# Performance work log

Hardware: AMD Instinct MI355X
Metric: run time of the kernel (lower is better)

## Reference

```python
import jax, jax.numpy as jnp
import numpy as np

# ---- static config (matches init_kwargs) ----
NLAT, NLON = 181, 360
LMAX = NLAT                 # hard_thresholding_fraction = 1.0
MMAX = NLON // 2 + 1        # 181, real FFT in longitude
INC = 26
OUTC = 26
EMBED = 256
NLAYERS = 4
MLP_HID = int(EMBED * 2.0)
EPS = 1e-6


def _legendre(lmax, mmax, theta):
    """Orthonormal associated Legendre functions Pbar[l, m, k] at colatitudes theta."""
    ct, st = np.cos(theta), np.sin(theta)
    K = theta.size
    P = np.zeros((lmax, mmax, K), dtype=np.float64)
    P[0, 0] = np.sqrt(1.0 / (4.0 * np.pi))
    for m in range(1, mmax):
        P[m, m] = -np.sqrt((2.0 * m + 1.0) / (2.0 * m)) * st * P[m - 1, m - 1]
    for m in range(mmax):
        if m + 1 < lmax:
            P[m + 1, m] = np.sqrt(2.0 * m + 3.0) * ct * P[m, m]
        for l in range(m + 2, lmax):
            a = np.sqrt((4.0 * l * l - 1.0) / (l * l - m * m))
            b = np.sqrt(((2.0 * l + 1.0) * (l - 1.0 + m) * (l - 1.0 - m)) / ((2.0 * l - 3.0) * (l * l - m * m)))
            P[l, m] = a * ct * P[l - 1, m] - b * P[l - 2, m]
    return P

# equiangular grid + quadrature weights; precompute analysis/synthesis matrices
_theta = np.linspace(0.0, np.pi, NLAT)
_wq = (np.pi / (NLAT - 1)) * np.sin(_theta)
_P = _legendre(LMAX, MMAX, _theta)
PW = jnp.asarray((_P * (2.0 * np.pi * _wq)[None, None, :]).astype(np.float32))  # analysis
PS = jnp.asarray(_P.astype(np.float32))                                         # synthesis


def _ln(x):
    # per-pixel layer norm over channel dim, no affine (affine_norms=False)
    mu = jnp.mean(x, axis=1, keepdims=True)
    var = jnp.mean((x - mu) ** 2, axis=1, keepdims=True)
    return (x - mu) * jax.lax.rsqrt(var + EPS)


def _conv1x1(x, w, b=None):
    y = jnp.einsum('oi,bihw->bohw', w, x)
    return y if b is None else y + b[None, :, None, None]


def _sht(x):
    # x: (b,c,nlat,nlon) -> coeff (b,c,l,m) complex64
    F = jnp.fft.rfft(x, axis=-1) / NLON          # (b,c,k,m)
    return jnp.einsum('lmk,bckm->bclm', PW, F)


def _isht(c):
    F = jnp.einsum('lmk,bclm->bckm', PS, c)      # (b,c,k,m)
    return jnp.fft.irfft(F * NLON, n=NLON, axis=-1)


def _block(x, wsp, bsp, wis, bis, wf1, bf1, wf2, bf2):
    xn = _ln(x)                                  # norm0
    c = _sht(xn)
    co = jnp.einsum('oil,bilm->bolm', wsp, c)    # dhconv: diagonal in m, dense per l
    y = _isht(co) + bsp[None, :, None, None]
    x1 = y + _conv1x1(xn, wis, bis)              # inner linear skip (residual = filter input)
    x1 = jax.nn.gelu(x1, approximate=False)
    x2 = _ln(x1)                                 # norm1
    h = jax.nn.gelu(_conv1x1(x2, wf1, bf1), approximate=False)
    x2 = _conv1x1(h, wf2, bf2)                   # MLP
    return x2 + xn                               # outer identity skip


def setup_inputs() -> dict:
    key = jax.random.key(0)
    ks = jax.random.split(key, 10)
    n = jax.random.normal
    x = n(ks[0], (1, INC, NLAT, NLON), jnp.float32)
    w_enc = n(ks[1], (EMBED, INC), jnp.float32) * float(1.0 / np.sqrt(INC))
    b_enc = jnp.zeros((EMBED,), jnp.float32)
    pos_emb = n(ks[2], (1, EMBED, NLAT, NLON), jnp.float32) * 0.02
    w_spec = n(ks[3], (NLAYERS, EMBED, EMBED, LMAX), jnp.float32) * float(1.0 / np.sqrt(EMBED))
    b_spec = jnp.zeros((NLAYERS, EMBED), jnp.float32)
    w_iskip = n(ks[4], (NLAYERS, EMBED, EMBED), jnp.float32) * float(1.0 / np.sqrt(EMBED))
    b_iskip = jnp.zeros((NLAYERS, EMBED), jnp.float32)
    w_fc1 = n(ks[5], (NLAYERS, MLP_HID, EMBED), jnp.float32) * float(1.0 / np.sqrt(EMBED))
    b_fc1 = jnp.zeros((NLAYERS, MLP_HID), jnp.float32)
    w_fc2 = n(ks[6], (NLAYERS, EMBED, MLP_HID), jnp.float32) * float(1.0 / np.sqrt(MLP_HID))
    b_fc2 = jnp.zeros((NLAYERS, EMBED), jnp.float32)
    w_dec = n(ks[7], (OUTC, EMBED + INC), jnp.float32) * float(1.0 / np.sqrt(EMBED + INC))
    b_dec = jnp.zeros((OUTC,), jnp.float32)
    return {'x': x, 'w_enc': w_enc, 'b_enc': b_enc, 'pos_emb': pos_emb,
            'w_spec': w_spec, 'b_spec': b_spec, 'w_iskip': w_iskip, 'b_iskip': b_iskip,
            'w_fc1': w_fc1, 'b_fc1': b_fc1, 'w_fc2': w_fc2, 'b_fc2': b_fc2,
            'w_dec': w_dec, 'b_dec': b_dec}


def reference(x, w_enc, b_enc, pos_emb, w_spec, b_spec, w_iskip, b_iskip,
              w_fc1, b_fc1, w_fc2, b_fc2, w_dec, b_dec):
    res = x                                       # big_skip residual (raw input)
    h = _conv1x1(x, w_enc, b_enc) + pos_emb       # encoder + pos embed
    for i in range(NLAYERS):
        h = _block(h, w_spec[i], b_spec[i], w_iskip[i], b_iskip[i],
                   w_fc1[i], b_fc1[i], w_fc2[i], b_fc2[i])
    h = jnp.concatenate([h, res], axis=1)         # big skip concat
    return _conv1x1(h, w_dec, b_dec)
```

## Files before the change

kernel.cpp:

```cpp
#include <hip/hip_runtime.h>
#include <math.h>

#define NLATg 181
#define NLONg 360
#define PIXg  65160
#define EMBg  256
#define MHIDg 512
#define PLANEg 8386816
#define LDIMg 32761

#define FLAG_GELU 1
#define FLAG_ACC  2

__device__ __forceinline__ float gelu_f(float x) {
    return 0.5f * x * (1.0f + erff(x * 0.70710678118654752440f));
}


__global__ __launch_bounds__(256) void init_legendre(float* __restrict__ P) {
    int idx = blockIdx.x * 256 + threadIdx.x;
    if (idx >= 181 * 181) return;
    int m = idx / 181, k = idx % 181;
    double theta = M_PI * (double)k / 180.0;
    double ct = cos(theta), st = sin(theta);
    double pmm = sqrt(1.0 / (4.0 * M_PI));
    for (int j = 1; j <= m; ++j) pmm *= -sqrt((2.0 * j + 1.0) / (2.0 * j)) * st;
    for (int l = 0; l < m; ++l) P[(size_t)l * LDIMg + m * 181 + k] = 0.0f;
    P[(size_t)m * LDIMg + m * 181 + k] = (float)pmm;
    if (m + 1 < 181) {
        double pl1 = sqrt(2.0 * m + 3.0) * ct * pmm;
        P[(size_t)(m + 1) * LDIMg + m * 181 + k] = (float)pl1;
        double pl2 = pmm;
        for (int l = m + 2; l < 181; ++l) {
            double ll = l, mm = m;
            double a = sqrt((4.0 * ll * ll - 1.0) / (ll * ll - mm * mm));
            double b = sqrt(((2.0 * ll + 1.0) * (ll - 1.0 + mm) * (ll - 1.0 - mm)) /
                            ((2.0 * ll - 3.0) * (ll * ll - mm * mm)));
            double p = a * ct * pl1 - b * pl2;
            P[(size_t)l * LDIMg + m * 181 + k] = (float)p;
            pl2 = pl1; pl1 = p;
        }
    }
}

__global__ __launch_bounds__(256) void init_trig(float* __restrict__ Etrig,
                                                 float* __restrict__ Dt, float* __restrict__ wqs) {
    int idx = blockIdx.x * 256 + threadIdx.x;
    if (idx < 181) {
        double theta = M_PI * (double)idx / 180.0;
        wqs[idx] = (float)(2.0 * M_PI * (M_PI / 180.0) * sin(theta) / 360.0);
    }
    if (idx >= 181 * 360) return;
    int m = idx / 360, n = idx % 360;
    int a = (m * n) % 360;
    double ang = M_PI * (double)a / 180.0;
    double c = cos(ang), s = sin(ang);
    Etrig[idx]         = (float)c;
    Etrig[PIXg + idx]  = (float)(-s);
    double cm = (m == 0 || m == 180) ? 1.0 : 2.0;
    Dt[(size_t)m * 360 + n]         = (float)(cm * c);
    Dt[(size_t)(181 + m) * 360 + n] = (float)(-cm * s);
}

__global__ __launch_bounds__(256) void transpose_wspec(const float* __restrict__ W, float* __restrict__ WT) {
    __shared__ float tile[32][33];
    int l0 = blockIdx.x * 32, o0 = blockIdx.y * 32, i = blockIdx.z;
    int c = threadIdx.x & 31, r = threadIdx.x >> 5;
#pragma unroll
    for (int j = 0; j < 4; j++) {
        int row = r + j * 8;
        float v = 0.f;
        if (l0 + c < 181) v = W[(size_t)(o0 + row) * 46336 + i * 181 + (l0 + c)];
        tile[row][c] = v;
    }
    __syncthreads();
#pragma unroll
    for (int j = 0; j < 4; j++) {
        int row = r + j * 8;
        if (l0 + row < 181) WT[(size_t)(l0 + row) * 65536 + i * 256 + (o0 + c)] = tile[c][row];
    }
}

__global__ __launch_bounds__(256) void ln_kernel(const float* __restrict__ X, float* __restrict__ Y) {
    int p0 = blockIdx.x * 64;
    int t = threadIdx.x;
    int ps = t & 63, cg = t >> 6;
    int p = p0 + ps;
    bool ok = p < PIXg;
    float sum = 0.f, sumsq = 0.f;
    if (ok) {
        for (int c = cg; c < EMBg; c += 4) {
            float v = X[(size_t)c * PIXg + p];
            sum += v; sumsq += v * v;
        }
    }
    __shared__ float s1[4][64];
    __shared__ float s2[4][64];
    s1[cg][ps] = sum; s2[cg][ps] = sumsq;
    __syncthreads();
    float tot  = s1[0][ps] + s1[1][ps] + s1[2][ps] + s1[3][ps];
    float tot2 = s2[0][ps] + s2[1][ps] + s2[2][ps] + s2[3][ps];
    float mu = tot * (1.0f / 256.0f);
    float var = tot2 * (1.0f / 256.0f) - mu * mu;
    float inv = rsqrtf(var + 1e-6f);
    if (ok) {
        for (int c = cg; c < EMBg; c += 4) {
            size_t offp = (size_t)c * PIXg + p;
            Y[offp] = (X[offp] - mu) * inv;
        }
    }
}

__global__ __launch_bounds__(256) void add_bias_gelu(const float* __restrict__ Y, const float* __restrict__ S,
                                                     const float* __restrict__ bsp, float* __restrict__ O) {
    int idx = blockIdx.x * 256 + threadIdx.x;
    int c = idx / 16290;
    float b = bsp[c];
    float4 y = reinterpret_cast<const float4*>(Y)[idx];
    float4 s = reinterpret_cast<const float4*>(S)[idx];
    float4 o;
    o.x = gelu_f(y.x + s.x + b);
    o.y = gelu_f(y.y + s.y + b);
    o.z = gelu_f(y.z + s.z + b);
    o.w = gelu_f(y.w + s.w + b);
    reinterpret_cast<float4*>(O)[idx] = o;
}

__global__ __launch_bounds__(256, 2) void gemm_f32(
    const float* __restrict__ A, int Ars, int Acs, int Azs, int Aps,
    const float* __restrict__ B, int Brs, int Bcs, int Bzs, int Bps,
    float* __restrict__ C, int Crs, int Ccs, int Czs, int Cps,
    const float* __restrict__ bias, const float* __restrict__ zscale,
    const float* __restrict__ resid,
    int M, int N, int K, int Zin, int flags)
{
    int z = blockIdx.z;
    if (z >= Zin) { z -= Zin; A += Aps; B += Bps; C += Cps; if (resid) resid += Cps; }
    A += (size_t)z * Azs; B += (size_t)z * Bzs; C += (size_t)z * Czs;
    if (resid) resid += (size_t)z * Czs;

    const int bm = blockIdx.y * 128, bn = blockIdx.x * 128;
    const int t = threadIdx.x;
    const int tx = t & 15, ty = t >> 4;

    __shared__ float As[16][132];
    __shared__ float Bs[16][132];

    float acc[8][8];
#pragma unroll
    for (int i = 0; i < 8; i++)
#pragma unroll
        for (int j = 0; j < 8; j++) acc[i][j] = 0.0f;

    for (int k0 = 0; k0 < K; k0 += 16) {
        if (Acs == 1) {
            int kk = t & 15, r = t >> 4;
            int gk = k0 + kk; bool kv = gk < K;
#pragma unroll
            for (int i = 0; i < 8; i++) {
                int gr = bm + r + i * 16; if (gr > M - 1) gr = M - 1;
                As[kk][r + i * 16] = kv ? A[(size_t)gr * Ars + gk] : 0.f;
            }
        } else {
            int row = t & 127, kb = t >> 7;
            int gr = bm + row; if (gr > M - 1) gr = M - 1;
            size_t base = (size_t)gr * Ars;
#pragma unroll
            for (int i = 0; i < 8; i++) {
                int gk = k0 + kb + i * 2;
                As[kb + i * 2][row] = (gk < K) ? A[base + (size_t)gk * Acs] : 0.f;
            }
        }
        if (Bcs == 1) {
            int col = t & 127, kb = t >> 7;
            int gc = bn + col; if (gc > N - 1) gc = N - 1;
#pragma unroll
            for (int i = 0; i < 8; i++) {
                int gk = k0 + kb + i * 2;
                Bs[kb + i * 2][col] = (gk < K) ? B[(size_t)gk * Brs + gc] : 0.f;
            }
        } else {
            int kk = t & 15, cb = t >> 4;
            int gk = k0 + kk; bool kv = gk < K;
#pragma unroll
            for (int i = 0; i < 8; i++) {
                int gc = bn + cb + i * 16; if (gc > N - 1) gc = N - 1;
                Bs[kk][cb + i * 16] = kv ? B[(size_t)gk * Brs + (size_t)gc * Bcs] : 0.f;
            }
        }
        __syncthreads();
#pragma unroll
        for (int kk = 0; kk < 16; kk++) {
            float4 a0 = *(const float4*)&As[kk][ty * 4];
            float4 a1 = *(const float4*)&As[kk][ty * 4 + 64];
            float4 b0 = *(const float4*)&Bs[kk][tx * 4];
            float4 b1 = *(const float4*)&Bs[kk][tx * 4 + 64];
            float av[8] = {a0.x, a0.y, a0.z, a0.w, a1.x, a1.y, a1.z, a1.w};
            float bv[8] = {b0.x, b0.y, b0.z, b0.w, b1.x, b1.y, b1.z, b1.w};
#pragma unroll
            for (int i = 0; i < 8; i++)
#pragma unroll
                for (int j = 0; j < 8; j++)
                    acc[i][j] = fmaf(av[i], bv[j], acc[i][j]);
        }
        __syncthreads();
    }

    const float zs = zscale ? zscale[z] : 1.0f;
    const bool fastN = (Ccs == 1) && (bn + 128 <= N);
#pragma unroll
    for (int i = 0; i < 8; i++) {
        int gi = bm + ty * 4 + (i & 3) + ((i >> 2) << 6);
        if (gi >= M) continue;
        float bval = bias ? bias[gi] : 0.0f;
        size_t crow = (size_t)gi * (size_t)Crs;
        if (fastN) {
#pragma unroll
            for (int h = 0; h < 2; h++) {
                int gj = bn + tx * 4 + h * 64;
                size_t off = crow + (size_t)gj;
                float4 v;
                v.x = acc[i][h * 4 + 0] * zs + bval;
                v.y = acc[i][h * 4 + 1] * zs + bval;
                v.z = acc[i][h * 4 + 2] * zs + bval;
                v.w = acc[i][h * 4 + 3] * zs + bval;
                if (resid) { float4 r = *(const float4*)&resid[off];
                             v.x += r.x; v.y += r.y; v.z += r.z; v.w += r.w; }
                if (flags & FLAG_GELU) { v.x = gelu_f(v.x); v.y = gelu_f(v.y);
                                         v.z = gelu_f(v.z); v.w = gelu_f(v.w); }
                if (flags & FLAG_ACC)  { float4 c0 = *(const float4*)&C[off];
                                         v.x += c0.x; v.y += c0.y; v.z += c0.z; v.w += c0.w; }
                *(float4*)&C[off] = v;
            }
        } else {
#pragma unroll
            for (int j = 0; j < 8; j++) {
                int gj = bn + tx * 4 + (j & 3) + ((j >> 2) << 6);
                if (gj >= N) continue;
                size_t off = crow + (size_t)gj * (size_t)Ccs;
                float v = acc[i][j] * zs + bval;
                if (resid) v += resid[off];
                if (flags & FLAG_GELU) v = gelu_f(v);
                if (flags & FLAG_ACC) v += C[off];
                C[off] = v;
            }
        }
    }
}

static inline void launch_gemm(hipStream_t s,
    const float* A, int Ars, int Acs, int Azs, int Aps,
    const float* B, int Brs, int Bcs, int Bzs, int Bps,
    float* C, int Crs, int Ccs, int Czs, int Cps,
    const float* bias, const float* zscale, const float* resid,
    int M, int N, int K, int Zin, int nplanes, int flags)
{
    dim3 grid((N + 127) / 128, (M + 127) / 128, Zin * nplanes);
    hipLaunchKernelGGL(gemm_f32, grid, dim3(256), 0, s,
                       A, Ars, Acs, Azs, Aps, B, Brs, Bcs, Bzs, Bps,
                       C, Crs, Ccs, Czs, Cps, bias, zscale, resid,
                       M, N, K, Zin, flags);
}

extern "C" void kernel_launch(void* const* d_in, const int* in_sizes, int n_in,
                              void* d_out, int out_size, void* d_ws, size_t ws_size,
                              hipStream_t stream)
{
    const float* x      = (const float*)d_in[0];
    const float* w_enc  = (const float*)d_in[1];
    const float* b_enc  = (const float*)d_in[2];
    const float* pos    = (const float*)d_in[3];
    const float* w_spec = (const float*)d_in[4];
    const float* b_spec = (const float*)d_in[5];
    const float* w_is   = (const float*)d_in[6];
    const float* b_is   = (const float*)d_in[7];
    const float* w_f1   = (const float*)d_in[8];
    const float* b_f1   = (const float*)d_in[9];
    const float* w_f2   = (const float*)d_in[10];
    const float* b_f2   = (const float*)d_in[11];
    const float* w_dec  = (const float*)d_in[12];
    const float* b_dec  = (const float*)d_in[13];
    float* out = (float*)d_out;
    float* ws  = (float*)d_ws;

    size_t off = 0;
    auto alloc = [&](size_t n) { size_t o = off; off += (n + 63) & ~(size_t)63; return o; };
    float* P     = ws + alloc((size_t)181 * 181 * 181);
    float* Etrig = ws + alloc((size_t)2 * PIXg);
    float* Dt    = ws + alloc((size_t)362 * 360);
    float* wqs   = ws + alloc(181);
    float* S0    = ws + alloc((size_t)2 * PLANEg);
    float* S1    = ws + alloc((size_t)2 * PLANEg);
    float* hbuf  = ws + alloc((size_t)EMBg * PIXg);
    float* xn    = ws + alloc((size_t)EMBg * PIXg);
    float* tA    = ws + alloc((size_t)EMBg * PIXg);
    float* tB    = ws + alloc((size_t)EMBg * PIXg);
    float* hmlp  = S0;

    init_legendre<<<(181 * 181 + 255) / 256, 256, 0, stream>>>(P);
    init_trig<<<(181 * 360 + 255) / 256, 256, 0, stream>>>(Etrig, Dt, wqs);

    launch_gemm(stream, w_enc, 26, 1, 0, 0,  x, PIXg, 1, 0, 0,  hbuf, PIXg, 1, 0, 0,
                b_enc, nullptr, pos, EMBg, PIXg, 26, 1, 1, 0);

    for (int L = 0; L < 4; ++L) {
        const float* wsp = w_spec + (size_t)L * EMBg * EMBg * 181;
        const float* bsp = b_spec + (size_t)L * EMBg;
        const float* wis = w_is   + (size_t)L * EMBg * EMBg;
        const float* bis = b_is   + (size_t)L * EMBg;
        const float* wf1 = w_f1   + (size_t)L * MHIDg * EMBg;
        const float* bf1 = b_f1   + (size_t)L * MHIDg;
        const float* wf2 = w_f2   + (size_t)L * EMBg * MHIDg;
        const float* bf2 = b_f2   + (size_t)L * EMBg;

        transpose_wspec<<<dim3(6, 8, 256), 256, 0, stream>>>(wsp, tA);

        ln_kernel<<<1019, 256, 0, stream>>>(hbuf, xn);

        launch_gemm(stream, Etrig, 360, 1, 0, PIXg,  xn, 1, PIXg, 360, 0,
                    S0, 256, 1, 46336, PLANEg,
                    nullptr, wqs, nullptr, 181, 256, 360, 181, 2, 0);
        launch_gemm(stream, P, LDIMg, 1, 181, 0,  S0, 46336, 1, 256, PLANEg,
                    S1, 256, 1, 46336, PLANEg,
                    nullptr, nullptr, nullptr, 181, 256, 181, 181, 2, 0);
        launch_gemm(stream, S1, 46336, 1, 256, PLANEg,  tA, 256, 1, 65536, 0,
                    S0, 46336, 1, 256, PLANEg,
                    nullptr, nullptr, nullptr, 181, 256, 256, 181, 2, 0);
        launch_gemm(stream, P, 1, LDIMg, 181, 0,  S0, 256, 1, 46336, PLANEg,
                    S1, 256, 1, 46336, PLANEg,
                    nullptr, nullptr, nullptr, 181, 256, 181, 181, 2, 0);
        launch_gemm(stream, S1, 1, 46336, 256, 0,  Dt, 360, 1, 0, 0,
                    tA, PIXg, 1, 360, 0,
                    nullptr, nullptr, nullptr, 256, 360, 362, 181, 1, 0);
        launch_gemm(stream, wis, 256, 1, 0, 0,  xn, PIXg, 1, 0, 0,  tB, PIXg, 1, 0, 0,
                    bis, nullptr, nullptr, 256, PIXg, 256, 1, 1, 0);
        add_bias_gelu<<<16290, 256, 0, stream>>>(tA, tB, bsp, tA);
        ln_kernel<<<1019, 256, 0, stream>>>(tA, tB);
        launch_gemm(stream, wf1, 256, 1, 0, 0,  tB, PIXg, 1, 0, 0,  hmlp, PIXg, 1, 0, 0,
                    bf1, nullptr, nullptr, MHIDg, PIXg, 256, 1, 1, FLAG_GELU);
        launch_gemm(stream, wf2, 512, 1, 0, 0,  hmlp, PIXg, 1, 0, 0,  hbuf, PIXg, 1, 0, 0,
                    bf2, nullptr, xn, EMBg, PIXg, 512, 1, 1, 0);
    }

    launch_gemm(stream, w_dec, 282, 1, 0, 0,  hbuf, PIXg, 1, 0, 0,  out, PIXg, 1, 0, 0,
                b_dec, nullptr, nullptr, 26, PIXg, 256, 1, 1, 0);
    launch_gemm(stream, w_dec + 256, 282, 1, 0, 0,  x, PIXg, 1, 0, 0,  out, PIXg, 1, 0, 0,
                nullptr, nullptr, nullptr, 26, PIXg, 26, 1, 1, FLAG_ACC);
}
```

Before: 10.73 ms.

## Replace FP32 GEMMs with split-BF16 MFMA GEMMs using hi/lo operand pairs

Adds a bf16 MFMA GEMM kernel that emulates fp32 accuracy with three products (hi*hi, hi*lo, lo*hi). All precomputed tables, weights, layer-norm outputs and spectral intermediates are stored as split bf16 hi/lo pairs. The inner-skip GEMM now accumulates directly into the spectral output, which removes a separate add pass and one buffer. The aim is to move the FP32 SIMT GEMM work onto matrix cores, at the cost of extra split kernels, three MFMAs per tile and some loss of precision.

Result: slower. 18.77 ms (+74.9%).

```diff
diff --git a/kernel.cpp b/kernel.cpp
--- a/kernel.cpp
+++ b/kernel.cpp
@@ -7,17 +7,32 @@
 #define EMBg  256
 #define MHIDg 512
 #define PLANEg 8386816
-#define LDIMg 32761
+#define PMSTRg 182
+#define PLSTRg 32942
 
 #define FLAG_GELU 1
 #define FLAG_ACC  2
+#define FLAG_F32  4
+#define FLAG_BF16 8
+
+typedef unsigned short u16;
+typedef unsigned int   u32;
+typedef __attribute__((ext_vector_type(8))) short bf16x8;
+typedef __attribute__((ext_vector_type(4))) float f32x4;
 
 __device__ __forceinline__ float gelu_f(float x) {
     return 0.5f * x * (1.0f + erff(x * 0.70710678118654752440f));
 }
 
-
-__global__ __launch_bounds__(256) void init_legendre(float* __restrict__ P) {
+__device__ __forceinline__ void split_f(float v, u16& h, u16& l) {
+    u32 u = __float_as_uint(v);
+    h = (u16)(u >> 16);
+    float hf = __uint_as_float(u & 0xFFFF0000u);
+    l = (u16)(__float_as_uint(v - hf) >> 16);
+}
+
+
+__global__ __launch_bounds__(256) void init_legendre(u16* __restrict__ Ph, u16* __restrict__ Pl) {
     int idx = blockIdx.x * 256 + threadIdx.x;
     if (idx >= 181 * 181) return;
     int m = idx / 181, k = idx % 181;
@@ -25,26 +40,35 @@
     double ct = cos(theta), st = sin(theta);
     double pmm = sqrt(1.0 / (4.0 * M_PI));
     for (int j = 1; j <= m; ++j) pmm *= -sqrt((2.0 * j + 1.0) / (2.0 * j)) * st;
-    for (int l = 0; l < m; ++l) P[(size_t)l * LDIMg + m * 181 + k] = 0.0f;
-    P[(size_t)m * LDIMg + m * 181 + k] = (float)pmm;
+    u16 h, l;
+    for (int l2 = 0; l2 < m; ++l2) {
+        size_t o = (size_t)l2 * PLSTRg + m * PMSTRg + k;
+        Ph[o] = 0; Pl[o] = 0;
+    }
+    split_f((float)pmm, h, l);
+    { size_t o = (size_t)m * PLSTRg + m * PMSTRg + k; Ph[o] = h; Pl[o] = l; }
     if (m + 1 < 181) {
         double pl1 = sqrt(2.0 * m + 3.0) * ct * pmm;
-        P[(size_t)(m + 1) * LDIMg + m * 181 + k] = (float)pl1;
+        split_f((float)pl1, h, l);
+        { size_t o = (size_t)(m + 1) * PLSTRg + m * PMSTRg + k; Ph[o] = h; Pl[o] = l; }
         double pl2 = pmm;
-        for (int l = m + 2; l < 181; ++l) {
-            double ll = l, mm = m;
-            double a = sqrt((4.0 * ll * ll - 1.0) / (ll * ll - mm * mm));
-            double b = sqrt(((2.0 * ll + 1.0) * (ll - 1.0 + mm) * (ll - 1.0 - mm)) /
-                            ((2.0 * ll - 3.0) * (ll * ll - mm * mm)));
+        for (int ll = m + 2; ll < 181; ++ll) {
+            double L = ll, M2 = m;
+            double a = sqrt((4.0 * L * L - 1.0) / (L * L - M2 * M2));
+            double b = sqrt(((2.0 * L + 1.0) * (L - 1.0 + M2) * (L - 1.0 - M2)) /
+                            ((2.0 * L - 3.0) * (L * L - M2 * M2)));
             double p = a * ct * pl1 - b * pl2;
-            P[(size_t)l * LDIMg + m * 181 + k] = (float)p;
+            split_f((float)p, h, l);
+            size_t o = (size_t)ll * PLSTRg + m * PMSTRg + k;
+            Ph[o] = h; Pl[o] = l;
             pl2 = pl1; pl1 = p;
         }
     }
 }
 
-__global__ __launch_bounds__(256) void init_trig(float* __restrict__ Etrig,
-                                                 float* __restrict__ Dt, float* __restrict__ wqs) {
+__global__ __launch_bounds__(256) void init_trig(u16* __restrict__ Eh, u16* __restrict__ El,
+                                                 u16* __restrict__ Dth, u16* __restrict__ Dtl,
+                                                 float* __restrict__ wqs) {
     int idx = blockIdx.x * 256 + threadIdx.x;
     if (idx < 181) {
         double theta = M_PI * (double)idx / 180.0;
@@ -55,14 +79,18 @@
     int a = (m * n) % 360;
     double ang = M_PI * (double)a / 180.0;
     double c = cos(ang), s = sin(ang);
-    Etrig[idx]         = (float)c;
-    Etrig[PIXg + idx]  = (float)(-s);
+    u16 h, l;
+    split_f((float)c, h, l);        Eh[idx] = h;        El[idx] = l;
+    split_f((float)(-s), h, l);     Eh[PIXg + idx] = h; El[PIXg + idx] = l;
     double cm = (m == 0 || m == 180) ? 1.0 : 2.0;
-    Dt[(size_t)m * 360 + n]         = (float)(cm * c);
-    Dt[(size_t)(181 + m) * 360 + n] = (float)(-cm * s);
-}
-
-__global__ __launch_bounds__(256) void transpose_wspec(const float* __restrict__ W, float* __restrict__ WT) {
+    split_f((float)(cm * c), h, l);
+    Dth[(size_t)m * 360 + n] = h;          Dtl[(size_t)m * 360 + n] = l;
+    split_f((float)(-cm * s), h, l);
+    Dth[(size_t)(181 + m) * 360 + n] = h;  Dtl[(size_t)(181 + m) * 360 + n] = l;
+}
+
+__global__ __launch_bounds__(256) void transpose_wspec(const float* __restrict__ W,
+                                                       u16* __restrict__ WTh, u16* __restrict__ WTl) {
     __shared__ float tile[32][33];
     int l0 = blockIdx.x * 32, o0 = blockIdx.y * 32, i = blockIdx.z;
     int c = threadIdx.x & 31, r = threadIdx.x >> 5;
@@ -77,11 +105,24 @@
 #pragma unroll
     for (int j = 0; j < 4; j++) {
         int row = r + j * 8;
-        if (l0 + row < 181) WT[(size_t)(l0 + row) * 65536 + i * 256 + (o0 + c)] = tile[c][row];
-    }
-}
-
-__global__ __launch_bounds__(256) void ln_kernel(const float* __restrict__ X, float* __restrict__ Y) {
+        if (l0 + row < 181) {
+            u16 h, l; split_f(tile[c][row], h, l);
+            size_t o = (size_t)(l0 + row) * 65536 + i * 256 + (o0 + c);
+            WTh[o] = h; WTl[o] = l;
+        }
+    }
+}
+
+__global__ __launch_bounds__(256) void split_bf16(const float* __restrict__ in,
+                                                  u16* __restrict__ h, u16* __restrict__ l, int n) {
+    int i = blockIdx.x * 256 + threadIdx.x;
+    if (i >= n) return;
+    u16 hh, ll; split_f(in[i], hh, ll);
+    h[i] = hh; l[i] = ll;
+}
+
+__global__ __launch_bounds__(256) void ln_kernel(const float* __restrict__ X, float* __restrict__ Y,
+                                                 u16* __restrict__ Yh, u16* __restrict__ Yl) {
     int p0 = blockIdx.x * 64;
     int t = threadIdx.x;
     int ps = t & 63, cg = t >> 6;
@@ -106,24 +147,22 @@
     if (ok) {
         for (int c = cg; c < EMBg; c += 4) {
             size_t offp = (size_t)c * PIXg + p;
-            Y[offp] = (X[offp] - mu) * inv;
-        }
-    }
-}
-
-__global__ __launch_bounds__(256) void add_bias_gelu(const float* __restrict__ Y, const float* __restrict__ S,
-                                                     const float* __restrict__ bsp, float* __restrict__ O) {
+            float v = (X[offp] - mu) * inv;
+            if (Y) Y[offp] = v;
+            u16 h, l; split_f(v, h, l);
+            Yh[offp] = h; Yl[offp] = l;
+        }
+    }
+}
+
+__global__ __launch_bounds__(256) void gelu_bias(float* __restrict__ X, const float* __restrict__ b) {
     int idx = blockIdx.x * 256 + threadIdx.x;
     int c = idx / 16290;
-    float b = bsp[c];
-    float4 y = reinterpret_cast<const float4*>(Y)[idx];
-    float4 s = reinterpret_cast<const float4*>(S)[idx];
-    float4 o;
-    o.x = gelu_f(y.x + s.x + b);
-    o.y = gelu_f(y.y + s.y + b);
-    o.z = gelu_f(y.z + s.z + b);
-    o.w = gelu_f(y.w + s.w + b);
-    reinterpret_cast<float4*>(O)[idx] = o;
+    float bv = b[c];
+    float4 v = reinterpret_cast<float4*>(X)[idx];
+    v.x = gelu_f(v.x + bv); v.y = gelu_f(v.y + bv);
+    v.z = gelu_f(v.z + bv); v.w = gelu_f(v.w + bv);
+    reinterpret_cast<float4*>(X)[idx] = v;
 }
 
 __global__ __launch_bounds__(256, 2) void gemm_f32(
@@ -248,6 +287,203 @@
     }
 }
 
+__global__ __launch_bounds__(256, 2) void gemm_bf16(
+    const u16* __restrict__ Ah, const u16* __restrict__ Al,
+    int Ars, int Acs, int Azs, int Aps,
+    const u16* __restrict__ Bh, const u16* __restrict__ Bl,
+    int Brs, int Bcs, int Bzs, int Bps,
+    float* __restrict__ C, u16* __restrict__ Ch, u16* __restrict__ Cl,
+    int Crs, int Ccs, int Czs, int Cps,
+    const float* __restrict__ bias, const float* __restrict__ zscale,
+    const float* __restrict__ resid,
+    int M, int N, int K, int Zin, int flags)
+{
+    int z = blockIdx.z;
+    if (z >= Zin) {
+        z -= Zin;
+        Ah += Aps; Al += Aps; Bh += Bps; Bl += Bps;
+        if (C) C += Cps;
+        if (Ch) Ch += Cps;
+        if (Cl) Cl += Cps;
+        if (resid) resid += Cps;
+    }
+    Ah += (size_t)z * Azs; Al += (size_t)z * Azs;
+    Bh += (size_t)z * Bzs; Bl += (size_t)z * Bzs;
+    const size_t czoff = (size_t)z * Czs;
+
+    const int t = threadIdx.x;
+    const int lane = t & 63;
+    const int bm = blockIdx.y * 128, bn = blockIdx.x * 128;
+
+    __shared__ u16 Ahs[128 * 40];
+    __shared__ u16 Als[128 * 40];
+    __shared__ u16 Bhs[128 * 40];
+    __shared__ u16 Bls[128 * 40];
+
+    f32x4 acc[4][4];
+#pragma unroll
+    for (int i = 0; i < 4; i++)
+#pragma unroll
+        for (int j = 0; j < 4; j++) acc[i][j] = (f32x4){0.f, 0.f, 0.f, 0.f};
+
+    const int wid = t >> 6;
+    const int wm = (wid >> 1) * 64, wn = (wid & 1) * 64;
+    const int fr = lane & 15, fgb = lane >> 4;
+
+    int aoff[4], boff[4];
+#pragma unroll
+    for (int f = 0; f < 4; f++) {
+        int ra = wm + f * 16 + fr;
+        aoff[f] = ra * 40 + (((fgb ^ (ra >> 3)) & 3) << 3);
+        int rb = wn + f * 16 + fr;
+        boff[f] = rb * 40 + (((fgb ^ (rb >> 3)) & 3) << 3);
+    }
+
+    for (int k0 = 0; k0 < K; k0 += 32) {
+        if (Acs == 1) {
+            int kk = (t & 15) * 2;
+            int rg = t >> 4;
+            int gk = k0 + kk;
+            bool p2 = (gk + 1 < K), p1 = (gk < K);
+#pragma unroll
+            for (int i = 0; i < 8; i++) {
+                int r = rg + 16 * i;
+                int gr = bm + r; if (gr > M - 1) gr = M - 1;
+                size_t o = (size_t)gr * Ars + gk;
+                u32 vh = 0, vl = 0;
+                if (p2)      { vh = *(const u32*)(Ah + o); vl = *(const u32*)(Al + o); }
+                else if (p1) { vh = Ah[o]; vl = Al[o]; }
+                int so = r * 40 + ((((kk >> 3) ^ (r >> 3)) & 3) << 3) + (kk & 7);
+                *(u32*)(Ahs + so) = vh;
+                *(u32*)(Als + so) = vl;
+            }
+        } else {
+            int ml = (t & 63) * 2;
+            int kg = t >> 6;
+            int gr0 = bm + ml;     if (gr0 > M - 1) gr0 = M - 1;
+            int gr1 = bm + ml + 1; if (gr1 > M - 1) gr1 = M - 1;
+            bool pair = (gr1 == gr0 + 1);
+#pragma unroll
+            for (int i = 0; i < 8; i++) {
+                int kk = kg + 4 * i;
+                int gk = k0 + kk;
+                u32 vh = 0, vl = 0;
+                if (gk < K) {
+                    size_t o = (size_t)gk * Acs + gr0;
+                    if (pair) { vh = *(const u32*)(Ah + o); vl = *(const u32*)(Al + o); }
+                    else {
+                        vh = Ah[o]; vl = Al[o];
+                        u32 h1 = Ah[(size_t)gk * Acs + gr1], l1 = Al[(size_t)gk * Acs + gr1];
+                        vh |= h1 << 16; vl |= l1 << 16;
+                    }
+                }
+                int blk = (kk >> 3) & 3;
+                int s0 = ml * 40 + (((blk ^ (ml >> 3)) & 3) << 3) + (kk & 7);
+                int s1 = (ml + 1) * 40 + (((blk ^ ((ml + 1) >> 3)) & 3) << 3) + (kk & 7);
+                Ahs[s0] = (u16)vh; Ahs[s1] = (u16)(vh >> 16);
+                Als[s0] = (u16)vl; Als[s1] = (u16)(vl >> 16);
+            }
+        }
+        if (Bcs == 1) {
+            int jl = (t & 63) * 2;
+            int kg = t >> 6;
+            int gj0 = bn + jl;     if (gj0 > N - 1) gj0 = N - 1;
+            int gj1 = bn + jl + 1; if (gj1 > N - 1) gj1 = N - 1;
+            bool pair = (gj1 == gj0 + 1);
+#pragma unroll
+            for (int i = 0; i < 8; i++) {
+                int kk = kg + 4 * i;
+                int gk = k0 + kk;
+                u32 vh = 0, vl = 0;
+                if (gk < K) {
+                    size_t o = (size_t)gk * Brs + gj0;
+                    if (pair) { vh = *(const u32*)(Bh + o); vl = *(const u32*)(Bl + o); }
+                    else {
+                        vh = Bh[o]; vl = Bl[o];
+                        u32 h1 = Bh[(size_t)gk * Brs + gj1], l1 = Bl[(size_t)gk * Brs + gj1];
+                        vh |= h1 << 16; vl |= l1 << 16;
+                    }
+                }
+                int blk = (kk >> 3) & 3;
+                int s0 = jl * 40 + (((blk ^ (jl >> 3)) & 3) << 3) + (kk & 7);
+                int s1 = (jl + 1) * 40 + (((blk ^ ((jl + 1) >> 3)) & 3) << 3) + (kk & 7);
+                Bhs[s0] = (u16)vh; Bhs[s1] = (u16)(vh >> 16);
+                Bls[s0] = (u16)vl; Bls[s1] = (u16)(vl >> 16);
+            }
+        } else {
+            int kk = (t & 15) * 2;
+            int jg = t >> 4;
+            int gk = k0 + kk;
+            bool p2 = (gk + 1 < K), p1 = (gk < K);
+#pragma unroll
+            for (int i = 0; i < 8; i++) {
+                int j = jg + 16 * i;
+                int gj = bn + j; if (gj > N - 1) gj = N - 1;
+                size_t o = (size_t)gj * Bcs + gk;
+                u32 vh = 0, vl = 0;
+                if (p2)      { vh = *(const u32*)(Bh + o); vl = *(const u32*)(Bl + o); }
+                else if (p1) { vh = Bh[o]; vl = Bl[o]; }
+                int so = j * 40 + ((((kk >> 3) ^ (j >> 3)) & 3) << 3) + (kk & 7);
+                *(u32*)(Bhs + so) = vh;
+                *(u32*)(Bls + so) = vl;
+            }
+        }
+        __syncthreads();
+
+        bf16x8 fah[4], fal[4], fbh[4], fbl[4];
+#pragma unroll
+        for (int f = 0; f < 4; f++) {
+            fah[f] = *(const bf16x8*)(Ahs + aoff[f]);
+            fal[f] = *(const bf16x8*)(Als + aoff[f]);
+            fbh[f] = *(const bf16x8*)(Bhs + boff[f]);
+            fbl[f] = *(const bf16x8*)(Bls + boff[f]);
+        }
+#pragma unroll
+        for (int i = 0; i < 4; i++)
+#pragma unroll
+            for (int j = 0; j < 4; j++)
+                acc[i][j] = __builtin_amdgcn_mfma_f32_16x16x32_bf16(fah[i], fbh[j], acc[i][j], 0, 0, 0);
+#pragma unroll
+        for (int i = 0; i < 4; i++)
+#pragma unroll
+            for (int j = 0; j < 4; j++)
+                acc[i][j] = __builtin_amdgcn_mfma_f32_16x16x32_bf16(fah[i], fbl[j], acc[i][j], 0, 0, 0);
+#pragma unroll
+        for (int i = 0; i < 4; i++)
+#pragma unroll
+            for (int j = 0; j < 4; j++)
+                acc[i][j] = __builtin_amdgcn_mfma_f32_16x16x32_bf16(fal[i], fbh[j], acc[i][j], 0, 0, 0);
+        __syncthreads();
+    }
+
+    const float zs = zscale ? zscale[z] : 1.0f;
+#pragma unroll
+    for (int i = 0; i < 4; i++) {
+#pragma unroll
+        for (int r = 0; r < 4; r++) {
+            int grow = bm + wm + i * 16 + (lane >> 4) * 4 + r;
+            if (grow >= M) continue;
+            float bval = bias ? bias[grow] : 0.0f;
+            size_t rowoff = czoff + (size_t)grow * Crs;
+#pragma unroll
+            for (int j = 0; j < 4; j++) {
+                int gcol = bn + wn + j * 16 + fr;
+                if (gcol >= N) continue;
+                size_t off = rowoff + (size_t)gcol * Ccs;
+                float v = acc[i][j][r] * zs + bval;
+                if (resid) v += resid[off];
+                if (flags & FLAG_ACC) v += C[off];
+                if (flags & FLAG_GELU) v = gelu_f(v);
+                if (flags & FLAG_F32) C[off] = v;
+                if (flags & FLAG_BF16) {
+                    u16 h, l; split_f(v, h, l);
+                    Ch[off] = h; Cl[off] = l;
+                }
+            }
+        }
+    }
+}
+
 static inline void launch_gemm(hipStream_t s,
     const float* A, int Ars, int Acs, int Azs, int Aps,
     const float* B, int Brs, int Bcs, int Bzs, int Bps,
@@ -259,6 +495,20 @@
     hipLaunchKernelGGL(gemm_f32, grid, dim3(256), 0, s,
                        A, Ars, Acs, Azs, Aps, B, Brs, Bcs, Bzs, Bps,
                        C, Crs, Ccs, Czs, Cps, bias, zscale, resid,
+                       M, N, K, Zin, flags);
+}
+
+static inline void launch_gemm16(hipStream_t s,
+    const u16* Ah, const u16* Al, int Ars, int Acs, int Azs, int Aps,
+    const u16* Bh, const u16* Bl, int Brs, int Bcs, int Bzs, int Bps,
+    float* C, u16* Ch, u16* Cl, int Crs, int Ccs, int Czs, int Cps,
+    const float* bias, const float* zscale, const float* resid,
+    int M, int N, int K, int Zin, int nplanes, int flags)
+{
+    dim3 grid((N + 127) / 128, (M + 127) / 128, Zin * nplanes);
+    hipLaunchKernelGGL(gemm_bf16, grid, dim3(256), 0, s,
+                       Ah, Al, Ars, Acs, Azs, Aps, Bh, Bl, Brs, Bcs, Bzs, Bps,
+                       C, Ch, Cl, Crs, Ccs, Czs, Cps, bias, zscale, resid,
                        M, N, K, Zin, flags);
 }
 
@@ -281,24 +531,40 @@
     const float* w_dec  = (const float*)d_in[12];
     const float* b_dec  = (const float*)d_in[13];
     float* out = (float*)d_out;
-    float* ws  = (float*)d_ws;
-
+
+    char* base = (char*)d_ws;
     size_t off = 0;
-    auto alloc = [&](size_t n) { size_t o = off; off += (n + 63) & ~(size_t)63; return o; };
-    float* P     = ws + alloc((size_t)181 * 181 * 181);
-    float* Etrig = ws + alloc((size_t)2 * PIXg);
-    float* Dt    = ws + alloc((size_t)362 * 360);
-    float* wqs   = ws + alloc(181);
-    float* S0    = ws + alloc((size_t)2 * PLANEg);
-    float* S1    = ws + alloc((size_t)2 * PLANEg);
-    float* hbuf  = ws + alloc((size_t)EMBg * PIXg);
-    float* xn    = ws + alloc((size_t)EMBg * PIXg);
-    float* tA    = ws + alloc((size_t)EMBg * PIXg);
-    float* tB    = ws + alloc((size_t)EMBg * PIXg);
-    float* hmlp  = S0;
-
-    init_legendre<<<(181 * 181 + 255) / 256, 256, 0, stream>>>(P);
-    init_trig<<<(181 * 360 + 255) / 256, 256, 0, stream>>>(Etrig, Dt, wqs);
+    auto alloc = [&](size_t bytes) { size_t o = off; off += (bytes + 255) & ~(size_t)255; return o; };
+    u16* Ph  = (u16*)(base + alloc(11925004));
+    u16* Pl  = (u16*)(base + alloc(11925004));
+    u16* Eh  = (u16*)(base + alloc(260640));
+    u16* El  = (u16*)(base + alloc(260640));
+    u16* Dth = (u16*)(base + alloc(260640));
+    u16* Dtl = (u16*)(base + alloc(260640));
+    float* wqs = (float*)(base + alloc(724));
+    u16* SP  = (u16*)(base + alloc(134189056));
+    u16* S0h = SP;
+    u16* S0l = SP + 16773632;
+    u16* S1h = SP + 2 * 16773632;
+    u16* S1l = SP + 3 * 16773632;
+    u16* hmlph = SP;
+    u16* hmlpl = SP + 33361920;
+    float* xn  = (float*)(base + alloc(66723840));
+    u16* xnh = (u16*)(base + alloc(33361920));
+    u16* xnl = (u16*)(base + alloc(33361920));
+    float* hbuf = (float*)(base + alloc(66723840));
+    float* tA   = (float*)(base + alloc(66723840));
+    u16* wth = (u16*)tA;
+    u16* wtl = wth + 11862016;
+    u16* wish = (u16*)(base + alloc(131072));
+    u16* wisl = (u16*)(base + alloc(131072));
+    u16* wf1h = (u16*)(base + alloc(262144));
+    u16* wf1l = (u16*)(base + alloc(262144));
+    u16* wf2h = (u16*)(base + alloc(262144));
+    u16* wf2l = (u16*)(base + alloc(262144));
+
+    init_legendre<<<(181 * 181 + 255) / 256, 256, 0, stream>>>(Ph, Pl);
+    init_trig<<<(181 * 360 + 255) / 256, 256, 0, stream>>>(Eh, El, Dth, Dtl, wqs);
 
     launch_gemm(stream, w_enc, 26, 1, 0, 0,  x, PIXg, 1, 0, 0,  hbuf, PIXg, 1, 0, 0,
                 b_enc, nullptr, pos, EMBg, PIXg, 26, 1, 1, 0);
@@ -313,33 +579,39 @@
         const float* wf2 = w_f2   + (size_t)L * EMBg * MHIDg;
         const float* bf2 = b_f2   + (size_t)L * EMBg;
 
-        transpose_wspec<<<dim3(6, 8, 256), 256, 0, stream>>>(wsp, tA);
-
-        ln_kernel<<<1019, 256, 0, stream>>>(hbuf, xn);
-
-        launch_gemm(stream, Etrig, 360, 1, 0, PIXg,  xn, 1, PIXg, 360, 0,
-                    S0, 256, 1, 46336, PLANEg,
-                    nullptr, wqs, nullptr, 181, 256, 360, 181, 2, 0);
-        launch_gemm(stream, P, LDIMg, 1, 181, 0,  S0, 46336, 1, 256, PLANEg,
-                    S1, 256, 1, 46336, PLANEg,
-                    nullptr, nullptr, nullptr, 181, 256, 181, 181, 2, 0);
-        launch_gemm(stream, S1, 46336, 1, 256, PLANEg,  tA, 256, 1, 65536, 0,
-                    S0, 46336, 1, 256, PLANEg,
-                    nullptr, nullptr, nullptr, 181, 256, 256, 181, 2, 0);
-        launch_gemm(stream, P, 1, LDIMg, 181, 0,  S0, 256, 1, 46336, PLANEg,
-                    S1, 256, 1, 46336, PLANEg,
-                    nullptr, nullptr, nullptr, 181, 256, 181, 181, 2, 0);
-        launch_gemm(stream, S1, 1, 46336, 256, 0,  Dt, 360, 1, 0, 0,
-                    tA, PIXg, 1, 360, 0,
-                    nullptr, nullptr, nullptr, 256, 360, 362, 181, 1, 0);
-        launch_gemm(stream, wis, 256, 1, 0, 0,  xn, PIXg, 1, 0, 0,  tB, PIXg, 1, 0, 0,
-                    bis, nullptr, nullptr, 256, PIXg, 256, 1, 1, 0);
-        add_bias_gelu<<<16290, 256, 0, stream>>>(tA, tB, bsp, tA);
-        ln_kernel<<<1019, 256, 0, stream>>>(tA, tB);
-        launch_gemm(stream, wf1, 256, 1, 0, 0,  tB, PIXg, 1, 0, 0,  hmlp, PIXg, 1, 0, 0,
-                    bf1, nullptr, nullptr, MHIDg, PIXg, 256, 1, 1, FLAG_GELU);
-        launch_gemm(stream, wf2, 512, 1, 0, 0,  hmlp, PIXg, 1, 0, 0,  hbuf, PIXg, 1, 0, 0,
-                    bf2, nullptr, xn, EMBg, PIXg, 512, 1, 1, 0);
+        transpose_wspec<<<dim3(6, 8, 256), 256, 0, stream>>>(wsp, wth, wtl);
+        split_bf16<<<(65536 + 255) / 256, 256, 0, stream>>>(wis, wish, wisl, 65536);
+        split_bf16<<<(131072 + 255) / 256, 256, 0, stream>>>(wf1, wf1h, wf1l, 131072);
+        split_bf16<<<(131072 + 255) / 256, 256, 0, stream>>>(wf2, wf2h, wf2l, 131072);
+
+        ln_kernel<<<1019, 256, 0, stream>>>(hbuf, xn, xnh, xnl);
+
+        launch_gemm16(stream, Eh, El, 360, 1, 0, PIXg,  xnh, xnl, 1, PIXg, 360, 0,
+                      nullptr, S0h, S0l, 256, 1, 46336, PLANEg,
+                      nullptr, wqs, nullptr, 181, 256, 360, 181, 2, FLAG_BF16);
+        launch_gemm16(stream, Ph, Pl, PLSTRg, 1, PMSTRg, 0,  S0h, S0l, 46336, 1, 256, PLANEg,
+                      nullptr, S1h, S1l, 256, 1, 46336, PLANEg,
+                      nullptr, nullptr, nullptr, 181, 256, 181, 181, 2, FLAG_BF16);
+        launch_gemm16(stream, S1h, S1l, 46336, 1, 256, PLANEg,  wth, wtl, 256, 1, 65536, 0,
+                      nullptr, S0h, S0l, 46336, 1, 256, PLANEg,
+                      nullptr, nullptr, nullptr, 181, 256, 256, 181, 2, FLAG_BF16);
+        launch_gemm16(stream, Ph, Pl, 1, PLSTRg, PMSTRg, 0,  S0h, S0l, 256, 1, 46336, PLANEg,
+                      nullptr, S1h, S1l, 256, 1, 46336, PLANEg,
+                      nullptr, nullptr, nullptr, 181, 256, 181, 181, 2, FLAG_BF16);
+        launch_gemm16(stream, S1h, S1l, 1, 46336, 256, 0,  Dth, Dtl, 360, 1, 0, 0,
+                      tA, nullptr, nullptr, PIXg, 1, 360, 0,
+                      nullptr, nullptr, nullptr, 256, 360, 362, 181, 1, FLAG_F32);
+        launch_gemm16(stream, wish, wisl, 256, 1, 0, 0,  xnh, xnl, PIXg, 1, 0, 0,
+                      tA, nullptr, nullptr, PIXg, 1, 0, 0,
+                      bis, nullptr, nullptr, 256, PIXg, 256, 1, 1, FLAG_F32 | FLAG_ACC);
+        gelu_bias<<<16290, 256, 0, stream>>>(tA, bsp);
+        ln_kernel<<<1019, 256, 0, stream>>>(tA, nullptr, xnh, xnl);
+        launch_gemm16(stream, wf1h, wf1l, 256, 1, 0, 0,  xnh, xnl, PIXg, 1, 0, 0,
+                      nullptr, hmlph, hmlpl, PIXg, 1, 0, 0,
+                      bf1, nullptr, nullptr, MHIDg, PIXg, 256, 1, 1, FLAG_BF16 | FLAG_GELU);
+        launch_gemm16(stream, wf2h, wf2l, 512, 1, 0, 0,  hmlph, hmlpl, PIXg, 1, 0, 0,
+                      hbuf, nullptr, nullptr, PIXg, 1, 0, 0,
+                      bf2, nullptr, xn, EMBg, PIXg, 512, 1, 1, FLAG_F32);
     }
 
     launch_gemm(stream, w_dec, 282, 1, 0, 0,  hbuf, PIXg, 1, 0, 0,  out, PIXg, 1, 0, 0,
```
